# Performance work log

Hardware: AMD Instinct MI355X
Metric: run time of the kernel (lower is better)

The kernel has to match this reference:

```python
import jax, jax.numpy as jnp
import numpy as np

N_TOKENS = 32768
HIDDEN = 2048
NUM_EXPERTS = 64
TOP_K = 2


def setup_inputs() -> dict:
    key = jax.random.key(0)
    kx, kw = jax.random.split(key)
    x = jax.random.normal(kx, (N_TOKENS, HIDDEN), dtype=jnp.float32)
    # nn.Linear weight init scale ~ 1/sqrt(fan_in)
    gate_w = jax.random.normal(kw, (HIDDEN, NUM_EXPERTS), dtype=jnp.float32) / np.sqrt(HIDDEN)
    return {"x": x, "gate_w": gate_w}


def reference(x, gate_w):
    # logits: [N, E]
    logits = x @ gate_w
    # top-k over experts
    top_k_logits, top_k_indices = jax.lax.top_k(logits, TOP_K)  # [N, K]
    top_k_weights = jax.nn.softmax(top_k_logits, axis=-1)        # [N, K]
    probs = jax.nn.softmax(logits, axis=-1)                      # [N, E]
    # per-expert routed-token counts via segment-sum over flattened top-k indices
    tokens_per_expert = jax.ops.segment_sum(
        jnp.ones((x.shape[0] * TOP_K,), dtype=x.dtype),
        top_k_indices.reshape(-1),
        num_segments=NUM_EXPERTS,
    )
    f = tokens_per_expert / max(x.shape[0], 1)   # fraction of tokens per expert
    P = probs.mean(axis=0)                        # mean router prob per expert
    load_balance_loss = NUM_EXPERTS * jnp.sum(f * P)
    return top_k_weights, top_k_indices, load_balance_loss
```

## Files before the change

### kernel.cpp

```cpp
#include <hip/hip_runtime.h>
#include <math.h>

#define N_TOKENS 32768
#define HIDDEN   2048
#define NEXP     64
#define BM 64
#define NWAVE 4
#define NBLK (N_TOKENS / BM)
#define KSTEP 32
#define NSTEP 32
#define XSCALE 64.f
#define WSCALE 256.f
#define DESCALE (1.f / 16384.f)
#define NG 64

typedef __attribute__((ext_vector_type(8))) _Float16 half8;
typedef __attribute__((ext_vector_type(4))) float f32x4;

__global__ void wsplit_kernel(const float* __restrict__ gw,
                              _Float16* __restrict__ wh, _Float16* __restrict__ wl) {
    __shared__ float tile[KSTEP * NEXP];
    const int S   = blockIdx.x;
    const int tid = threadIdx.x;
    const float4* g4 = reinterpret_cast<const float4*>(gw + (size_t)S * KSTEP * NEXP);
    float4* t4 = reinterpret_cast<float4*>(tile);
    t4[tid]       = g4[tid];
    t4[tid + 256] = g4[tid + 256];
    __syncthreads();
    const int nt  = tid >> 6;
    const int l   = tid & 63;
    const int col = nt * 16 + (l & 15);
    const int kr  = (l >> 4) * 8;
    half8 vh, vl;
    #pragma unroll
    for (int j = 0; j < 8; ++j) {
        const float w = tile[(kr + j) * NEXP + col] * WSCALE;
        const _Float16 hh = (_Float16)w;
        vh[j] = hh;
        vl[j] = (_Float16)(w - (float)hh);
    }
    const size_t off = ((size_t)(S * 4 + nt) * 64 + l) * 8;
    *reinterpret_cast<half8*>(wh + off) = vh;
    *reinterpret_cast<half8*>(wl + off) = vl;
}

__global__ __launch_bounds__(256, 2)
void router_main(const float* __restrict__ x,
                 const _Float16* __restrict__ whp, const _Float16* __restrict__ wlp,
                 float* __restrict__ out_w, float* __restrict__ out_i,
                 float* __restrict__ wsP, int* __restrict__ wsC)
{
    __shared__ float part[2][BM][65];
    __shared__ float pred[NWAVE][NEXP];
    __shared__ int   cntl[NEXP];

    const int tid  = threadIdx.x;
    const int lane = tid & 63;
    const int wv   = tid >> 6;
    const int m0   = blockIdx.x * BM;
    if (tid < NEXP) cntl[tid] = 0;

    const int mrow = lane & 15;
    const int kq   = lane >> 4;
    const int wtok = (wv >> 1) * 32;
    const int kh   = wv & 1;
    const int Sb   = kh * NSTEP;

    const float* xb = x + (size_t)(m0 + wtok + mrow) * HIDDEN + (size_t)kh * 1024 + kq * 8;

    f32x4 a[4][2][2];
    half8 bh[2][4], bl[2][4];
    f32x4 acc[2][4];
    const f32x4 zero = {0.f, 0.f, 0.f, 0.f};
    #pragma unroll
    for (int mt = 0; mt < 2; ++mt)
        #pragma unroll
        for (int nt = 0; nt < 4; ++nt) acc[mt][nt] = zero;

    #define LOADA(SET, s_) {                                                          \
        _Pragma("unroll")                                                             \
        for (int mt = 0; mt < 2; ++mt) {                                              \
            const float* g_ = xb + (size_t)mt * (16 * HIDDEN) + (s_) * KSTEP;         \
            a[SET][mt][0] = *reinterpret_cast<const f32x4*>(g_);                      \
            a[SET][mt][1] = *reinterpret_cast<const f32x4*>(g_ + 4);                  \
        } }
    #define LOADB(SET, s_) {                                                          \
        const int S_ = Sb + (s_);                                                     \
        _Pragma("unroll")                                                             \
        for (int nt = 0; nt < 4; ++nt) {                                              \
            const size_t o_ = ((size_t)(S_ * 4 + nt) * 64 + lane) * 8;                \
            bh[SET][nt] = *reinterpret_cast<const half8*>(whp + o_);                  \
            bl[SET][nt] = *reinterpret_cast<const half8*>(wlp + o_);                  \
        } }
    #define COMPUTE(AS, BS) {                                                         \
        half8 ah[2], al[2];                                                           \
        _Pragma("unroll")                                                             \
        for (int mt = 0; mt < 2; ++mt)                                                \
            _Pragma("unroll")                                                         \
            for (int h = 0; h < 2; ++h)                                               \
                _Pragma("unroll")                                                     \
                for (int j = 0; j < 4; ++j) {                                         \
                    const float v_ = a[AS][mt][h][j] * XSCALE;                        \
                    const _Float16 hh_ = (_Float16)v_;                                \
                    ah[mt][h * 4 + j] = hh_;                                          \
                    al[mt][h * 4 + j] = (_Float16)(v_ - (float)hh_);                  \
                }                                                                     \
        _Pragma("unroll")                                                             \
        for (int mt = 0; mt < 2; ++mt)                                                \
            _Pragma("unroll")                                                         \
            for (int nt = 0; nt < 4; ++nt) {                                          \
                f32x4 c_ = acc[mt][nt];                                               \
                c_ = __builtin_amdgcn_mfma_f32_16x16x32_f16(ah[mt], bh[BS][nt], c_, 0, 0, 0); \
                c_ = __builtin_amdgcn_mfma_f32_16x16x32_f16(ah[mt], bl[BS][nt], c_, 0, 0, 0); \
                c_ = __builtin_amdgcn_mfma_f32_16x16x32_f16(al[mt], bh[BS][nt], c_, 0, 0, 0); \
                acc[mt][nt] = c_;                                                     \
            } }

    LOADA(0, 0); LOADA(1, 1); LOADA(2, 2); LOADB(0, 0);

    for (int t = 0; t < 7; ++t) {
        const int s = t * 4;
        LOADA(3, s + 3); LOADB(1, s + 1); COMPUTE(0, 0);
        LOADA(0, s + 4); LOADB(0, s + 2); COMPUTE(1, 1);
        LOADA(1, s + 5); LOADB(1, s + 3); COMPUTE(2, 0);
        LOADA(2, s + 6); LOADB(0, s + 4); COMPUTE(3, 1);
    }
    LOADA(3, 31); LOADB(1, 29); COMPUTE(0, 0);
    LOADB(0, 30); COMPUTE(1, 1);
    LOADB(1, 31); COMPUTE(2, 0);
    COMPUTE(3, 1);
    #undef LOADA
    #undef LOADB
    #undef COMPUTE

    #pragma unroll
    for (int mt = 0; mt < 2; ++mt)
        #pragma unroll
        for (int nt = 0; nt < 4; ++nt)
            #pragma unroll
            for (int r = 0; r < 4; ++r)
                part[kh][wtok + mt * 16 + (lane >> 4) * 4 + r][nt * 16 + (lane & 15)] =
                    acc[mt][nt][r] * DESCALE;
    __syncthreads();

    float sumP = 0.f;
    for (int t = 0; t < 16; ++t) {
        const int m = wv * 16 + t;
        const float l = part[0][m][lane] + part[1][m][lane];

        float v = l; int idx = lane;
        #pragma unroll
        for (int off = 32; off >= 1; off >>= 1) {
            float ov = __shfl_xor(v, off);
            int   oi = __shfl_xor(idx, off);
            if (ov > v || (ov == v && oi < idx)) { v = ov; idx = oi; }
        }
        const float v1 = v; const int i1 = idx;
        v = (lane == i1) ? -INFINITY : l;
        idx = lane;
        #pragma unroll
        for (int off = 32; off >= 1; off >>= 1) {
            float ov = __shfl_xor(v, off);
            int   oi = __shfl_xor(idx, off);
            if (ov > v || (ov == v && oi < idx)) { v = ov; idx = oi; }
        }
        const float v2 = v; const int i2 = idx;
        const float ed  = expf(v2 - v1);
        const float wt1 = 1.f / (1.f + ed);
        const float wt2 = ed / (1.f + ed);
        const float p = expf(l - v1);
        float Z = p;
        #pragma unroll
        for (int off = 32; off >= 1; off >>= 1) Z += __shfl_xor(Z, off);
        sumP += p / Z;
        if (lane == 0) {
            const size_t o = (size_t)(m0 + m) * 2;
            out_w[o]     = wt1;
            out_w[o + 1] = wt2;
            out_i[o]     = (float)i1;
            out_i[o + 1] = (float)i2;
            atomicAdd(&cntl[i1], 1);
            atomicAdd(&cntl[i2], 1);
        }
    }
    pred[wv][lane] = sumP;
    __syncthreads();
    if (tid < NEXP) {
        float s = 0.f;
        #pragma unroll
        for (int w2 = 0; w2 < NWAVE; ++w2) s += pred[w2][tid];
        wsP[(size_t)blockIdx.x * NEXP + tid] = s;
        wsC[(size_t)blockIdx.x * NEXP + tid] = cntl[tid];
    }
}

__global__ void router_fin1(const float* __restrict__ wsP, const int* __restrict__ wsC,
                            float* __restrict__ Ps1, float* __restrict__ Cs1)
{
    const int g = blockIdx.x;
    const int e = threadIdx.x;
    float P = 0.f, C = 0.f;
    #pragma unroll
    for (int r = 0; r < 8; ++r) {
        const size_t row = (size_t)(g * 8 + r) * NEXP + e;
        P += wsP[row];
        C += (float)wsC[row];
    }
    Ps1[(size_t)g * NEXP + e] = P;
    Cs1[(size_t)g * NEXP + e] = C;
}

__global__ void router_fin2(const float* __restrict__ Ps1, const float* __restrict__ Cs1,
                            float* __restrict__ out_loss)
{
    const int e = threadIdx.x;
    float P = 0.f, C = 0.f;
    #pragma unroll
    for (int g = 0; g < NG; ++g) {
        P += Ps1[(size_t)g * NEXP + e];
        C += Cs1[(size_t)g * NEXP + e];
    }
    float val = (C / (float)N_TOKENS) * (P / (float)N_TOKENS);
    #pragma unroll
    for (int off = 32; off >= 1; off >>= 1) val += __shfl_xor(val, off);
    if (e == 0) out_loss[0] = (float)NEXP * val;
}

extern "C" void kernel_launch(void* const* d_in, const int* in_sizes, int n_in,
                              void* d_out, int out_size, void* d_ws, size_t ws_size,
                              hipStream_t stream) {
    const float* x  = (const float*)d_in[0];
    const float* gw = (const float*)d_in[1];
    float* out   = (float*)d_out;
    float* out_w = out;
    float* out_i = out + (size_t)N_TOKENS * 2;
    float* loss  = out + (size_t)N_TOKENS * 4;
    float*    wsP = (float*)d_ws;
    int*      wsC = (int*)((char*)d_ws + 131072);
    _Float16* wh  = (_Float16*)((char*)d_ws + 262144);
    _Float16* wl  = wh + (size_t)HIDDEN * NEXP;
    float*    Ps1 = (float*)((char*)d_ws + 786432);
    float*    Cs1 = Ps1 + NG * NEXP;
    hipLaunchKernelGGL(wsplit_kernel, dim3(HIDDEN / KSTEP), dim3(256), 0, stream, gw, wh, wl);
    hipLaunchKernelGGL(router_main, dim3(NBLK), dim3(256), 0, stream,
                       x, wh, wl, out_w, out_i, wsP, wsC);
    hipLaunchKernelGGL(router_fin1, dim3(NG), dim3(64), 0, stream, wsP, wsC, Ps1, Cs1);
    hipLaunchKernelGGL(router_fin2, dim3(1), dim3(64), 0, stream, Ps1, Cs1, loss);
}
```

Baseline: 91.51 us.

## Use 8 waves per block with one 16-token tile per wave

Each 64-token block now runs 8 waves instead of 4, and each wave handles a single 16-row M-tile instead of two. The four-deep A-register prefetch becomes a two-deep double buffer, and launch bounds rise to 512 threads with 4 blocks per CU. This cuts per-wave register use and raises the number of waves in flight to hide global-load latency on the memory-bound x stream. The cost is that each wave now loads B fragments for half as many MFMAs, so B traffic per token doubles, and prefetch depth is shallower.

```diff
diff --git a/kernel.cpp b/kernel.cpp
--- a/kernel.cpp
+++ b/kernel.cpp
@@ -5,7 +5,7 @@
 #define HIDDEN   2048
 #define NEXP     64
 #define BM 64
-#define NWAVE 4
+#define NWAVE 8
 #define NBLK (N_TOKENS / BM)
 #define KSTEP 32
 #define NSTEP 32
@@ -44,7 +44,7 @@
     *reinterpret_cast<half8*>(wl + off) = vl;
 }
 
-__global__ __launch_bounds__(256, 2)
+__global__ __launch_bounds__(512, 4)
 void router_main(const float* __restrict__ x,
                  const _Float16* __restrict__ whp, const _Float16* __restrict__ wlp,
                  float* __restrict__ out_w, float* __restrict__ out_i,
@@ -62,28 +62,25 @@
 
     const int mrow = lane & 15;
     const int kq   = lane >> 4;
-    const int wtok = (wv >> 1) * 32;
+    const int tokg = wv >> 1;
     const int kh   = wv & 1;
     const int Sb   = kh * NSTEP;
 
-    const float* xb = x + (size_t)(m0 + wtok + mrow) * HIDDEN + (size_t)kh * 1024 + kq * 8;
-
-    f32x4 a[4][2][2];
+    const float* xb =
+        x + (size_t)(m0 + tokg * 16 + mrow) * HIDDEN + (size_t)kh * 1024 + kq * 8;
+
+    f32x4 a[2][2];
     half8 bh[2][4], bl[2][4];
-    f32x4 acc[2][4];
+    f32x4 acc[4];
     const f32x4 zero = {0.f, 0.f, 0.f, 0.f};
     #pragma unroll
-    for (int mt = 0; mt < 2; ++mt)
-        #pragma unroll
-        for (int nt = 0; nt < 4; ++nt) acc[mt][nt] = zero;
+    for (int nt = 0; nt < 4; ++nt) acc[nt] = zero;
 
     #define LOADA(SET, s_) {                                                          \
-        _Pragma("unroll")                                                             \
-        for (int mt = 0; mt < 2; ++mt) {                                              \
-            const float* g_ = xb + (size_t)mt * (16 * HIDDEN) + (s_) * KSTEP;         \
-            a[SET][mt][0] = *reinterpret_cast<const f32x4*>(g_);                      \
-            a[SET][mt][1] = *reinterpret_cast<const f32x4*>(g_ + 4);                  \
-        } }
+        const float* g_ = xb + (s_) * KSTEP;                                          \
+        a[SET][0] = *reinterpret_cast<const f32x4*>(g_);                              \
+        a[SET][1] = *reinterpret_cast<const f32x4*>(g_ + 4);                          \
+    }
     #define LOADB(SET, s_) {                                                          \
         const int S_ = Sb + (s_);                                                     \
         _Pragma("unroll")                                                             \
@@ -93,59 +90,49 @@
             bl[SET][nt] = *reinterpret_cast<const half8*>(wlp + o_);                  \
         } }
     #define COMPUTE(AS, BS) {                                                         \
-        half8 ah[2], al[2];                                                           \
+        half8 ah, al;                                                                 \
         _Pragma("unroll")                                                             \
-        for (int mt = 0; mt < 2; ++mt)                                                \
+        for (int h = 0; h < 2; ++h)                                                   \
             _Pragma("unroll")                                                         \
-            for (int h = 0; h < 2; ++h)                                               \
-                _Pragma("unroll")                                                     \
-                for (int j = 0; j < 4; ++j) {                                         \
-                    const float v_ = a[AS][mt][h][j] * XSCALE;                        \
-                    const _Float16 hh_ = (_Float16)v_;                                \
-                    ah[mt][h * 4 + j] = hh_;                                          \
-                    al[mt][h * 4 + j] = (_Float16)(v_ - (float)hh_);                  \
-                }                                                                     \
+            for (int j = 0; j < 4; ++j) {                                             \
+                const float v_ = a[AS][h][j] * XSCALE;                                \
+                const _Float16 hh_ = (_Float16)v_;                                    \
+                ah[h * 4 + j] = hh_;                                                  \
+                al[h * 4 + j] = (_Float16)(v_ - (float)hh_);                          \
+            }                                                                         \
         _Pragma("unroll")                                                             \
-        for (int mt = 0; mt < 2; ++mt)                                                \
-            _Pragma("unroll")                                                         \
-            for (int nt = 0; nt < 4; ++nt) {                                          \
-                f32x4 c_ = acc[mt][nt];                                               \
-                c_ = __builtin_amdgcn_mfma_f32_16x16x32_f16(ah[mt], bh[BS][nt], c_, 0, 0, 0); \
-                c_ = __builtin_amdgcn_mfma_f32_16x16x32_f16(ah[mt], bl[BS][nt], c_, 0, 0, 0); \
-                c_ = __builtin_amdgcn_mfma_f32_16x16x32_f16(al[mt], bh[BS][nt], c_, 0, 0, 0); \
-                acc[mt][nt] = c_;                                                     \
-            } }
-
-    LOADA(0, 0); LOADA(1, 1); LOADA(2, 2); LOADB(0, 0);
-
-    for (int t = 0; t < 7; ++t) {
-        const int s = t * 4;
-        LOADA(3, s + 3); LOADB(1, s + 1); COMPUTE(0, 0);
-        LOADA(0, s + 4); LOADB(0, s + 2); COMPUTE(1, 1);
-        LOADA(1, s + 5); LOADB(1, s + 3); COMPUTE(2, 0);
-        LOADA(2, s + 6); LOADB(0, s + 4); COMPUTE(3, 1);
-    }
-    LOADA(3, 31); LOADB(1, 29); COMPUTE(0, 0);
-    LOADB(0, 30); COMPUTE(1, 1);
-    LOADB(1, 31); COMPUTE(2, 0);
-    COMPUTE(3, 1);
+        for (int nt = 0; nt < 4; ++nt) {                                              \
+            f32x4 c_ = acc[nt];                                                       \
+            c_ = __builtin_amdgcn_mfma_f32_16x16x32_f16(ah, bh[BS][nt], c_, 0, 0, 0); \
+            c_ = __builtin_amdgcn_mfma_f32_16x16x32_f16(ah, bl[BS][nt], c_, 0, 0, 0); \
+            c_ = __builtin_amdgcn_mfma_f32_16x16x32_f16(al, bh[BS][nt], c_, 0, 0, 0); \
+            acc[nt] = c_;                                                             \
+        } }
+
+    LOADA(0, 0); LOADB(0, 0);
+
+    for (int t = 0; t < 16; ++t) {
+        const int s = t * 2;
+        LOADA(1, s + 1); LOADB(1, s + 1);
+        COMPUTE(0, 0);
+        if (s + 2 < NSTEP) { LOADA(0, s + 2); LOADB(0, s + 2); }
+        COMPUTE(1, 1);
+    }
     #undef LOADA
     #undef LOADB
     #undef COMPUTE
 
     #pragma unroll
-    for (int mt = 0; mt < 2; ++mt)
-        #pragma unroll
-        for (int nt = 0; nt < 4; ++nt)
-            #pragma unroll
-            for (int r = 0; r < 4; ++r)
-                part[kh][wtok + mt * 16 + (lane >> 4) * 4 + r][nt * 16 + (lane & 15)] =
-                    acc[mt][nt][r] * DESCALE;
+    for (int nt = 0; nt < 4; ++nt)
+        #pragma unroll
+        for (int r = 0; r < 4; ++r)
+            part[kh][tokg * 16 + (lane >> 4) * 4 + r][nt * 16 + (lane & 15)] =
+                acc[nt][r] * DESCALE;
     __syncthreads();
 
     float sumP = 0.f;
-    for (int t = 0; t < 16; ++t) {
-        const int m = wv * 16 + t;
+    for (int t = 0; t < 8; ++t) {
+        const int m = wv * 8 + t;
         const float l = part[0][m][lane] + part[1][m][lane];
 
         float v = l; int idx = lane;
@@ -242,7 +229,7 @@
     float*    Ps1 = (float*)((char*)d_ws + 786432);
     float*    Cs1 = Ps1 + NG * NEXP;
     hipLaunchKernelGGL(wsplit_kernel, dim3(HIDDEN / KSTEP), dim3(256), 0, stream, gw, wh, wl);
-    hipLaunchKernelGGL(router_main, dim3(NBLK), dim3(256), 0, stream,
+    hipLaunchKernelGGL(router_main, dim3(NBLK), dim3(512), 0, stream,
                        x, wh, wl, out_w, out_i, wsP, wsC);
     hipLaunchKernelGGL(router_fin1, dim3(NG), dim3(64), 0, stream, wsP, wsC, Ps1, Cs1);
     hipLaunchKernelGGL(router_fin2, dim3(1), dim3(64), 0, stream, Ps1, Cs1, loss);
```

New measurement: 112.9 us. 23.4% more time.

## Split hidden dim four ways across waves with smaller token blocks

Applied to the files above, without the earlier changes.

Each block now handles 32 tokens instead of 64, and its four waves each take a quarter of the hidden dimension rather than a half. Partial logits from the four waves are summed in shared memory. The A-load pipeline drops from four stages to double buffering, and launch bounds rise to three blocks per CU, doubling the grid to 1024 blocks. This is meant to raise occupancy and latency hiding for the memory-bound x stream, at the cost of more B-weight reloads per token and a larger shared partial buffer and workspace.

```diff
diff --git a/kernel.cpp b/kernel.cpp
--- a/kernel.cpp
+++ b/kernel.cpp
@@ -4,11 +4,11 @@
 #define N_TOKENS 32768
 #define HIDDEN   2048
 #define NEXP     64
-#define BM 64
+#define BM 32
 #define NWAVE 4
 #define NBLK (N_TOKENS / BM)
 #define KSTEP 32
-#define NSTEP 32
+#define NSTEP 16
 #define XSCALE 64.f
 #define WSCALE 256.f
 #define DESCALE (1.f / 16384.f)
@@ -44,13 +44,13 @@
     *reinterpret_cast<half8*>(wl + off) = vl;
 }
 
-__global__ __launch_bounds__(256, 2)
+__global__ __launch_bounds__(256, 3)
 void router_main(const float* __restrict__ x,
                  const _Float16* __restrict__ whp, const _Float16* __restrict__ wlp,
                  float* __restrict__ out_w, float* __restrict__ out_i,
                  float* __restrict__ wsP, int* __restrict__ wsC)
 {
-    __shared__ float part[2][BM][65];
+    __shared__ float part[NWAVE][BM][65];
     __shared__ float pred[NWAVE][NEXP];
     __shared__ int   cntl[NEXP];
 
@@ -62,13 +62,11 @@
 
     const int mrow = lane & 15;
     const int kq   = lane >> 4;
-    const int wtok = (wv >> 1) * 32;
-    const int kh   = wv & 1;
-    const int Sb   = kh * NSTEP;
-
-    const float* xb = x + (size_t)(m0 + wtok + mrow) * HIDDEN + (size_t)kh * 1024 + kq * 8;
-
-    f32x4 a[4][2][2];
+    const int Sb   = wv * NSTEP;
+
+    const float* xb = x + (size_t)(m0 + mrow) * HIDDEN + (size_t)wv * 512 + kq * 8;
+
+    f32x4 a[2][2][2];
     half8 bh[2][4], bl[2][4];
     f32x4 acc[2][4];
     const f32x4 zero = {0.f, 0.f, 0.f, 0.f};
@@ -116,19 +114,15 @@
                 acc[mt][nt] = c_;                                                     \
             } }
 
-    LOADA(0, 0); LOADA(1, 1); LOADA(2, 2); LOADB(0, 0);
-
-    for (int t = 0; t < 7; ++t) {
-        const int s = t * 4;
-        LOADA(3, s + 3); LOADB(1, s + 1); COMPUTE(0, 0);
-        LOADA(0, s + 4); LOADB(0, s + 2); COMPUTE(1, 1);
-        LOADA(1, s + 5); LOADB(1, s + 3); COMPUTE(2, 0);
-        LOADA(2, s + 6); LOADB(0, s + 4); COMPUTE(3, 1);
-    }
-    LOADA(3, 31); LOADB(1, 29); COMPUTE(0, 0);
-    LOADB(0, 30); COMPUTE(1, 1);
-    LOADB(1, 31); COMPUTE(2, 0);
-    COMPUTE(3, 1);
+    LOADA(0, 0); LOADB(0, 0);
+
+    for (int t = 0; t < NSTEP / 2; ++t) {
+        const int s = t * 2;
+        LOADA(1, s + 1); LOADB(1, s + 1);
+        COMPUTE(0, 0);
+        if (s + 2 < NSTEP) { LOADA(0, s + 2); LOADB(0, s + 2); }
+        COMPUTE(1, 1);
+    }
     #undef LOADA
     #undef LOADB
     #undef COMPUTE
@@ -139,14 +133,15 @@
         for (int nt = 0; nt < 4; ++nt)
             #pragma unroll
             for (int r = 0; r < 4; ++r)
-                part[kh][wtok + mt * 16 + (lane >> 4) * 4 + r][nt * 16 + (lane & 15)] =
+                part[wv][mt * 16 + (lane >> 4) * 4 + r][nt * 16 + (lane & 15)] =
                     acc[mt][nt][r] * DESCALE;
     __syncthreads();
 
     float sumP = 0.f;
-    for (int t = 0; t < 16; ++t) {
-        const int m = wv * 16 + t;
-        const float l = part[0][m][lane] + part[1][m][lane];
+    for (int t = 0; t < BM / NWAVE; ++t) {
+        const int m = wv * (BM / NWAVE) + t;
+        const float l = part[0][m][lane] + part[1][m][lane]
+                      + part[2][m][lane] + part[3][m][lane];
 
         float v = l; int idx = lane;
         #pragma unroll
@@ -201,8 +196,8 @@
     const int e = threadIdx.x;
     float P = 0.f, C = 0.f;
     #pragma unroll
-    for (int r = 0; r < 8; ++r) {
-        const size_t row = (size_t)(g * 8 + r) * NEXP + e;
+    for (int r = 0; r < NBLK / NG; ++r) {
+        const size_t row = (size_t)(g * (NBLK / NG) + r) * NEXP + e;
         P += wsP[row];
         C += (float)wsC[row];
     }
@@ -236,10 +231,10 @@
     float* out_i = out + (size_t)N_TOKENS * 2;
     float* loss  = out + (size_t)N_TOKENS * 4;
     float*    wsP = (float*)d_ws;
-    int*      wsC = (int*)((char*)d_ws + 131072);
-    _Float16* wh  = (_Float16*)((char*)d_ws + 262144);
+    int*      wsC = (int*)((char*)d_ws + 262144);
+    _Float16* wh  = (_Float16*)((char*)d_ws + 524288);
     _Float16* wl  = wh + (size_t)HIDDEN * NEXP;
-    float*    Ps1 = (float*)((char*)d_ws + 786432);
+    float*    Ps1 = (float*)((char*)d_ws + 1048576);
     float*    Cs1 = Ps1 + NG * NEXP;
     hipLaunchKernelGGL(wsplit_kernel, dim3(HIDDEN / KSTEP), dim3(256), 0, stream, gw, wh, wl);
     hipLaunchKernelGGL(router_main, dim3(NBLK), dim3(256), 0, stream,
```

Result: faster. 82.06 us (median of 3 runs) (-10.3%).
